# Kernel optimization log

Hardware: AMD Instinct MI355X
Metric: run time of the kernel (lower is better)

Reference implementation:

```python
import jax, jax.numpy as jnp
import numpy as np

B, S, D, H = 2, 2048, 1024, 16
HD = D // H
MASK_VALUE = -1000000.0


def setup_inputs() -> dict:
    key = jax.random.key(0)
    ks = jax.random.split(key, 8)
    scale = 1.0 / np.sqrt(D)
    return {
        "Q": jax.random.normal(ks[0], (B, S, D), jnp.float32),
        "K": jax.random.normal(ks[1], (B, S, D), jnp.float32),
        "V": jax.random.normal(ks[2], (B, S, D), jnp.float32),
        "valid_lens": jax.random.randint(ks[3], (B,), 0, S).astype(jnp.int32),
        "Wq": jax.random.normal(ks[4], (D, D), jnp.float32) * scale,
        "Wk": jax.random.normal(ks[5], (D, D), jnp.float32) * scale,
        "Wv": jax.random.normal(ks[6], (D, D), jnp.float32) * scale,
        "Wo": jax.random.normal(ks[7], (D, D), jnp.float32) * scale,
    }


def _split_heads(x):
    # [B,S,D] -> [B,H,S,HD]
    return x.reshape(B, S, H, HD).transpose(0, 2, 1, 3)


def reference(Q, K, V, valid_lens, Wq, Wk, Wv, Wo):
    q = _split_heads(Q @ Wq)
    k = _split_heads(K @ Wk)
    v = _split_heads(V @ Wv)
    # scores: [B,H,Sq,Sk]
    scores = jnp.einsum("bhqd,bhkd->bhqk", q, k) / jnp.sqrt(jnp.float32(HD))
    # mask key positions >= valid_len (per batch, broadcast over heads/queries)
    key_pos = jnp.arange(S)  # [Sk]
    mask = key_pos[None, None, None, :] < valid_lens[:, None, None, None]
    scores = jnp.where(mask, scores, MASK_VALUE)
    attn = jax.nn.softmax(scores, axis=-1)
    out = jnp.einsum("bhqk,bhkd->bhqd", attn, v)  # [B,H,S,HD]
    out = out.transpose(0, 2, 1, 3).reshape(B, S, D)
    return out @ Wo
```

## Files before the change

kernel.cpp:

```cpp
#include <hip/hip_runtime.h>
#include <stdint.h>

#define B_ 2
#define S_ 2048
#define D_ 1024
#define H_ 16
#define HD_ 64
#define MG_ (B_*S_)
#define MASKV -1000000.0f
#define LDA_ 72

typedef __bf16 bf16;
typedef bf16 bf16x8 __attribute__((ext_vector_type(8)));
typedef bf16 bf16x4 __attribute__((ext_vector_type(4)));
typedef float f32x4 __attribute__((ext_vector_type(4)));

#define MFMA(a, b, c) __builtin_amdgcn_mfma_f32_16x16x32_bf16(a, b, c, 0, 0, 0)

__global__ __launch_bounds__(256) void wcast_kernel(const float* __restrict__ W0, const float* __restrict__ W1,
                                                    const float* __restrict__ W2, const float* __restrict__ W3,
                                                    bf16* __restrict__ T) {
  const float* W = blockIdx.z == 0 ? W0 : blockIdx.z == 1 ? W1 : blockIdx.z == 2 ? W2 : W3;
  bf16* Tz = T + (size_t)blockIdx.z * D_ * D_;
  __shared__ float tile[32][33];
  int tx = threadIdx.x & 31, ty = threadIdx.x >> 5;
  int bn = blockIdx.x * 32, bk = blockIdx.y * 32;
#pragma unroll
  for (int i = 0; i < 32; i += 8)
    tile[ty + i][tx] = W[(size_t)(bk + ty + i) * D_ + bn + tx];
  __syncthreads();
#pragma unroll
  for (int i = 0; i < 32; i += 8)
    Tz[(size_t)(bn + ty + i) * D_ + bk + tx] = (bf16)tile[tx][ty + i];
}

__global__ __launch_bounds__(256) void proj_gemm(const float* __restrict__ Qin, const float* __restrict__ Kin,
                                                 const float* __restrict__ Vin, const bf16* __restrict__ WT,
                                                 bf16* __restrict__ qh, bf16* __restrict__ kh,
                                                 bf16* __restrict__ vT) {
  __shared__ alignas(16) bf16 As[128 * 32];
  __shared__ alignas(16) bf16 Bs[128 * 32];
  int mode = blockIdx.z;
  int tid = threadIdx.x, lane = tid & 63, w = tid >> 6;
  int wm = w >> 1, wn = w & 1, ml = lane & 15, quad = lane >> 4;
  int rr = tid >> 3, c4 = (tid & 7) * 4;
  f32x4 acc[4][4] = {};

  if (mode < 2) {
    const float* A = mode ? Kin : Qin;
    const bf16* Bt = WT + (size_t)mode * D_ * D_;
    bf16* dst = mode ? kh : qh;
    int m0 = blockIdx.y * 128, n0 = blockIdx.x * 128;
    for (int kk = 0; kk < D_; kk += 32) {
      __syncthreads();
#pragma unroll
      for (int p = 0; p < 4; ++p) {
        float4 v = *(const float4*)&A[(size_t)(m0 + rr + p * 32) * D_ + kk + c4];
        bf16x4 bv; bv[0] = (bf16)v.x; bv[1] = (bf16)v.y; bv[2] = (bf16)v.z; bv[3] = (bf16)v.w;
        *(bf16x4*)&As[(rr + p * 32) * 32 + c4] = bv;
      }
#pragma unroll
      for (int p = 0; p < 2; ++p) {
        int cc = tid + p * 256;
        int nr = cc >> 2, c8 = (cc & 3) * 8;
        *(bf16x8*)&Bs[nr * 32 + c8] = *(const bf16x8*)&Bt[(size_t)(n0 + nr) * D_ + kk + c8];
      }
      __syncthreads();
      bf16x8 af[4], bfr[4];
#pragma unroll
      for (int mt = 0; mt < 4; ++mt) af[mt] = *(bf16x8*)&As[(wm * 64 + mt * 16 + ml) * 32 + quad * 8];
#pragma unroll
      for (int nt = 0; nt < 4; ++nt) bfr[nt] = *(bf16x8*)&Bs[(wn * 64 + nt * 16 + ml) * 32 + quad * 8];
#pragma unroll
      for (int mt = 0; mt < 4; ++mt)
#pragma unroll
        for (int nt = 0; nt < 4; ++nt)
          acc[mt][nt] = MFMA(af[mt], bfr[nt], acc[mt][nt]);
    }
#pragma unroll
    for (int mt = 0; mt < 4; ++mt)
#pragma unroll
      for (int nt = 0; nt < 4; ++nt)
#pragma unroll
        for (int r = 0; r < 4; ++r) {
          int m = m0 + wm * 64 + mt * 16 + quad * 4 + r;
          int n = n0 + wn * 64 + nt * 16 + ml;
          int b = m >> 11, s = m & (S_ - 1), h = n >> 6, hd = n & 63;
          dst[(((size_t)(b * H_ + h)) * S_ + s) * HD_ + hd] = (bf16)acc[mt][nt][r];
        }
  } else {
    const bf16* At = WT + 2ull * D_ * D_;
    int m0 = blockIdx.x * 128;
    int n0 = blockIdx.y * 128;
    for (int kk = 0; kk < D_; kk += 32) {
      __syncthreads();
#pragma unroll
      for (int p = 0; p < 2; ++p) {
        int cc = tid + p * 256;
        int nr = cc >> 2, c8 = (cc & 3) * 8;
        *(bf16x8*)&As[nr * 32 + c8] = *(const bf16x8*)&At[(size_t)(m0 + nr) * D_ + kk + c8];
      }
#pragma unroll
      for (int p = 0; p < 4; ++p) {
        float4 v = *(const float4*)&Vin[(size_t)(n0 + rr + p * 32) * D_ + kk + c4];
        bf16x4 bv; bv[0] = (bf16)v.x; bv[1] = (bf16)v.y; bv[2] = (bf16)v.z; bv[3] = (bf16)v.w;
        *(bf16x4*)&Bs[(rr + p * 32) * 32 + c4] = bv;
      }
      __syncthreads();
      bf16x8 af[4], bfr[4];
#pragma unroll
      for (int mt = 0; mt < 4; ++mt) af[mt] = *(bf16x8*)&As[(wm * 64 + mt * 16 + ml) * 32 + quad * 8];
#pragma unroll
      for (int nt = 0; nt < 4; ++nt) bfr[nt] = *(bf16x8*)&Bs[(wn * 64 + nt * 16 + ml) * 32 + quad * 8];
#pragma unroll
      for (int mt = 0; mt < 4; ++mt)
#pragma unroll
        for (int nt = 0; nt < 4; ++nt)
          acc[mt][nt] = MFMA(af[mt], bfr[nt], acc[mt][nt]);
    }
#pragma unroll
    for (int mt = 0; mt < 4; ++mt)
#pragma unroll
      for (int nt = 0; nt < 4; ++nt)
#pragma unroll
        for (int r = 0; r < 4; ++r) {
          int dcol = m0 + wm * 64 + mt * 16 + quad * 4 + r;
          int n = n0 + wn * 64 + nt * 16 + ml;
          int b = n >> 11, s = n & (S_ - 1), h = dcol >> 6, hd = dcol & 63;
          vT[(((size_t)(b * H_ + h)) * HD_ + hd) * S_ + s] = (bf16)acc[mt][nt][r];
        }
  }
}

__global__ __launch_bounds__(256) void attn_kernel(const bf16* __restrict__ qh, const bf16* __restrict__ kh,
                                                   const bf16* __restrict__ vT, const int* __restrict__ vlen,
                                                   bf16* __restrict__ ctx) {
  __shared__ alignas(16) bf16 Qs[64 * LDA_];
  __shared__ alignas(16) bf16 Ks[64 * LDA_];
  __shared__ alignas(16) bf16 Vs[64 * LDA_];
  __shared__ alignas(16) bf16 Ps[4][16 * LDA_];
  int tid = threadIdx.x, lane = tid & 63, w = tid >> 6;
  int ml = lane & 15, quad = lane >> 4;
  int bh = blockIdx.y, b = bh >> 4, h = bh & 15;
  int qt = blockIdx.x;
  const bf16* qbase = qh + ((size_t)bh * S_ + qt * 64) * HD_;
  const bf16* kbase = kh + (size_t)bh * S_ * HD_;
  const bf16* vbase = vT + (size_t)bh * HD_ * S_;
  int valid = vlen[b];
  int nkt = (valid == 0) ? (S_ / 64) : ((valid + 63) >> 6);
  for (int c = tid; c < 64 * 8; c += 256) {
    int r = c >> 3, c8 = (c & 7) * 8;
    *(bf16x8*)&Qs[r * LDA_ + c8] = *(const bf16x8*)&qbase[r * 64 + c8];
  }
  float m_run[4] = {-1e30f, -1e30f, -1e30f, -1e30f};
  float l_run[4] = {0.f, 0.f, 0.f, 0.f};
  f32x4 o[4] = {};
  for (int kt = 0; kt < nkt; ++kt) {
    __syncthreads();
    for (int c = tid; c < 64 * 8; c += 256) {
      int r = c >> 3, c8 = (c & 7) * 8;
      *(bf16x8*)&Ks[r * LDA_ + c8] = *(const bf16x8*)&kbase[((size_t)kt * 64 + r) * HD_ + c8];
      *(bf16x8*)&Vs[r * LDA_ + c8] = *(const bf16x8*)&vbase[(size_t)r * S_ + kt * 64 + c8];
    }
    __syncthreads();
    bf16x8 aq0 = *(bf16x8*)&Qs[(w * 16 + ml) * LDA_ + quad * 8];
    bf16x8 aq1 = *(bf16x8*)&Qs[(w * 16 + ml) * LDA_ + 32 + quad * 8];
    f32x4 sc[4];
#pragma unroll
    for (int nt = 0; nt < 4; ++nt) {
      bf16x8 bk0 = *(bf16x8*)&Ks[(nt * 16 + ml) * LDA_ + quad * 8];
      bf16x8 bk1 = *(bf16x8*)&Ks[(nt * 16 + ml) * LDA_ + 32 + quad * 8];
      f32x4 c = {};
      c = MFMA(aq0, bk0, c);
      c = MFMA(aq1, bk1, c);
      sc[nt] = c;
    }
#pragma unroll
    for (int r = 0; r < 4; ++r) {
      float mx = -1e30f;
#pragma unroll
      for (int nt = 0; nt < 4; ++nt) {
        float s = sc[nt][r] * 0.125f;
        int col = kt * 64 + nt * 16 + ml;
        if (col >= valid) s = MASKV;
        sc[nt][r] = s;
        mx = fmaxf(mx, s);
      }
#pragma unroll
      for (int d = 1; d < 16; d <<= 1) mx = fmaxf(mx, __shfl_xor(mx, d));
      float mnew = fmaxf(m_run[r], mx);
      float ps = 0.f;
#pragma unroll
      for (int nt = 0; nt < 4; ++nt) {
        float p = __expf(sc[nt][r] - mnew);
        sc[nt][r] = p;
        ps += p;
      }
#pragma unroll
      for (int d = 1; d < 16; d <<= 1) ps += __shfl_xor(ps, d);
      float alpha = __expf(m_run[r] - mnew);
      l_run[r] = l_run[r] * alpha + ps;
      m_run[r] = mnew;
      o[0][r] *= alpha; o[1][r] *= alpha; o[2][r] *= alpha; o[3][r] *= alpha;
#pragma unroll
      for (int nt = 0; nt < 4; ++nt)
        Ps[w][(quad * 4 + r) * LDA_ + nt * 16 + ml] = (bf16)sc[nt][r];
    }
#pragma unroll
    for (int ks = 0; ks < 2; ++ks) {
      bf16x8 ap = *(bf16x8*)&Ps[w][ml * LDA_ + ks * 32 + quad * 8];
#pragma unroll
      for (int ht = 0; ht < 4; ++ht) {
        bf16x8 bv = *(bf16x8*)&Vs[(ht * 16 + ml) * LDA_ + ks * 32 + quad * 8];
        o[ht] = MFMA(ap, bv, o[ht]);
      }
    }
  }
#pragma unroll
  for (int r = 0; r < 4; ++r) {
    float inv = 1.0f / l_run[r];
    int s = qt * 64 + w * 16 + quad * 4 + r;
#pragma unroll
    for (int ht = 0; ht < 4; ++ht) {
      int d = h * 64 + ht * 16 + ml;
      ctx[((size_t)b * S_ + s) * D_ + d] = (bf16)(o[ht][r] * inv);
    }
  }
}

__global__ __launch_bounds__(256) void out_gemm(const bf16* __restrict__ ctx, const bf16* __restrict__ WoT,
                                                float* __restrict__ out) {
  __shared__ alignas(16) bf16 As[128 * 32];
  __shared__ alignas(16) bf16 Bs[64 * 32];
  int tid = threadIdx.x, lane = tid & 63, w = tid >> 6;
  int wm = w >> 1, wn = w & 1, ml = lane & 15, quad = lane >> 4;
  int m0 = blockIdx.y * 128, n0 = blockIdx.x * 64;
  f32x4 acc[4][2] = {};
  for (int kk = 0; kk < D_; kk += 32) {
    __syncthreads();
    {
#pragma unroll
      for (int p = 0; p < 2; ++p) {
        int cc = tid + p * 256;
        int nr = cc >> 2, c8 = (cc & 3) * 8;
        *(bf16x8*)&As[nr * 32 + c8] = *(const bf16x8*)&ctx[(size_t)(m0 + nr) * D_ + kk + c8];
      }
      int nr = tid >> 2, c8 = (tid & 3) * 8;
      *(bf16x8*)&Bs[nr * 32 + c8] = *(const bf16x8*)&WoT[(size_t)(n0 + nr) * D_ + kk + c8];
    }
    __syncthreads();
    bf16x8 af[4], bfr[2];
#pragma unroll
    for (int mt = 0; mt < 4; ++mt) af[mt] = *(bf16x8*)&As[(wm * 64 + mt * 16 + ml) * 32 + quad * 8];
#pragma unroll
    for (int nt = 0; nt < 2; ++nt) bfr[nt] = *(bf16x8*)&Bs[(wn * 32 + nt * 16 + ml) * 32 + quad * 8];
#pragma unroll
    for (int mt = 0; mt < 4; ++mt)
#pragma unroll
      for (int nt = 0; nt < 2; ++nt)
        acc[mt][nt] = MFMA(af[mt], bfr[nt], acc[mt][nt]);
  }
#pragma unroll
  for (int mt = 0; mt < 4; ++mt)
#pragma unroll
    for (int nt = 0; nt < 2; ++nt)
#pragma unroll
      for (int r = 0; r < 4; ++r) {
        int m = m0 + wm * 64 + mt * 16 + quad * 4 + r;
        int n = n0 + wn * 32 + nt * 16 + ml;
        out[(size_t)m * D_ + n] = acc[mt][nt][r];
      }
}

extern "C" void kernel_launch(void* const* d_in, const int* in_sizes, int n_in,
                              void* d_out, int out_size, void* d_ws, size_t ws_size,
                              hipStream_t stream) {
  const float* Q = (const float*)d_in[0];
  const float* K = (const float*)d_in[1];
  const float* V = (const float*)d_in[2];
  const int* vl = (const int*)d_in[3];
  const float* Wq = (const float*)d_in[4];
  const float* Wk = (const float*)d_in[5];
  const float* Wv = (const float*)d_in[6];
  const float* Wo = (const float*)d_in[7];
  char* ws = (char*)d_ws;
  bf16* WT  = (bf16*)ws;
  bf16* qh  = (bf16*)(ws + 8ull * 1024 * 1024);
  bf16* kh  = (bf16*)(ws + 16ull * 1024 * 1024);
  bf16* vT  = (bf16*)(ws + 24ull * 1024 * 1024);
  bf16* ctx = (bf16*)(ws + 32ull * 1024 * 1024);
  float* out = (float*)d_out;

  wcast_kernel<<<dim3(32, 32, 4), 256, 0, stream>>>(Wq, Wk, Wv, Wo, WT);
  proj_gemm<<<dim3(D_ / 128, MG_ / 128, 3), 256, 0, stream>>>(Q, K, V, WT, qh, kh, vT);
  attn_kernel<<<dim3(S_ / 64, B_ * H_), 256, 0, stream>>>(qh, kh, vT, vl, ctx);
  out_gemm<<<dim3(D_ / 64, MG_ / 128), 256, 0, stream>>>(ctx, WT + 3ull * D_ * D_, out);
}
```

Measured before the change: 249.7 us.

## Split attention key range across warps and merge partial softmax in LDS

The attention kernel now has each warp handle 32 query rows over half of the key tiles (even or odd), loading Q, K and V fragments straight from global memory into registers instead of staging them in shared memory with block-wide barriers. The per-warp partial outputs, maxima and sums are written to LDS at the end and combined split-k style. The 1/sqrt(d) scale is folded into the Q projection epilogue, and the mask check runs only on tail tiles. This removes the per-tile __syncthreads and LDS staging in exchange for redundant global K/V loads across warps and an extra merge step at the end.

```diff
diff --git a/kernel.cpp b/kernel.cpp
--- a/kernel.cpp
+++ b/kernel.cpp
@@ -8,7 +8,8 @@
 #define HD_ 64
 #define MG_ (B_*S_)
 #define MASKV -1000000.0f
-#define LDA_ 72
+#define LP_ 72
+#define LO_ 68
 
 typedef __bf16 bf16;
 typedef bf16 bf16x8 __attribute__((ext_vector_type(8)));
@@ -50,6 +51,7 @@
     const float* A = mode ? Kin : Qin;
     const bf16* Bt = WT + (size_t)mode * D_ * D_;
     bf16* dst = mode ? kh : qh;
+    float oscale = mode ? 1.0f : 0.125f;
     int m0 = blockIdx.y * 128, n0 = blockIdx.x * 128;
     for (int kk = 0; kk < D_; kk += 32) {
       __syncthreads();
@@ -86,7 +88,7 @@
           int m = m0 + wm * 64 + mt * 16 + quad * 4 + r;
           int n = n0 + wn * 64 + nt * 16 + ml;
           int b = m >> 11, s = m & (S_ - 1), h = n >> 6, hd = n & 63;
-          dst[(((size_t)(b * H_ + h)) * S_ + s) * HD_ + hd] = (bf16)acc[mt][nt][r];
+          dst[(((size_t)(b * H_ + h)) * S_ + s) * HD_ + hd] = (bf16)(acc[mt][nt][r] * oscale);
         }
   } else {
     const bf16* At = WT + 2ull * D_ * D_;
@@ -135,96 +137,136 @@
 __global__ __launch_bounds__(256) void attn_kernel(const bf16* __restrict__ qh, const bf16* __restrict__ kh,
                                                    const bf16* __restrict__ vT, const int* __restrict__ vlen,
                                                    bf16* __restrict__ ctx) {
-  __shared__ alignas(16) bf16 Qs[64 * LDA_];
-  __shared__ alignas(16) bf16 Ks[64 * LDA_];
-  __shared__ alignas(16) bf16 Vs[64 * LDA_];
-  __shared__ alignas(16) bf16 Ps[4][16 * LDA_];
+  __shared__ alignas(16) char ldsraw[35840];
+  bf16* Ps = (bf16*)ldsraw;
+  float* Om = (float*)ldsraw;
+  float* Mv = (float*)(ldsraw + 34816);
+  float* Lv = (float*)(ldsraw + 35328);
+
   int tid = threadIdx.x, lane = tid & 63, w = tid >> 6;
   int ml = lane & 15, quad = lane >> 4;
+  int wq = w >> 1, wk = w & 1;
   int bh = blockIdx.y, b = bh >> 4, h = bh & 15;
   int qt = blockIdx.x;
-  const bf16* qbase = qh + ((size_t)bh * S_ + qt * 64) * HD_;
+  const bf16* qbase = qh + ((size_t)bh * S_ + qt * 64 + wq * 32) * HD_;
   const bf16* kbase = kh + (size_t)bh * S_ * HD_;
   const bf16* vbase = vT + (size_t)bh * HD_ * S_;
   int valid = vlen[b];
   int nkt = (valid == 0) ? (S_ / 64) : ((valid + 63) >> 6);
-  for (int c = tid; c < 64 * 8; c += 256) {
-    int r = c >> 3, c8 = (c & 7) * 8;
-    *(bf16x8*)&Qs[r * LDA_ + c8] = *(const bf16x8*)&qbase[r * 64 + c8];
-  }
-  float m_run[4] = {-1e30f, -1e30f, -1e30f, -1e30f};
-  float l_run[4] = {0.f, 0.f, 0.f, 0.f};
-  f32x4 o[4] = {};
-  for (int kt = 0; kt < nkt; ++kt) {
-    __syncthreads();
-    for (int c = tid; c < 64 * 8; c += 256) {
-      int r = c >> 3, c8 = (c & 7) * 8;
-      *(bf16x8*)&Ks[r * LDA_ + c8] = *(const bf16x8*)&kbase[((size_t)kt * 64 + r) * HD_ + c8];
-      *(bf16x8*)&Vs[r * LDA_ + c8] = *(const bf16x8*)&vbase[(size_t)r * S_ + kt * 64 + c8];
-    }
-    __syncthreads();
-    bf16x8 aq0 = *(bf16x8*)&Qs[(w * 16 + ml) * LDA_ + quad * 8];
-    bf16x8 aq1 = *(bf16x8*)&Qs[(w * 16 + ml) * LDA_ + 32 + quad * 8];
-    f32x4 sc[4];
-#pragma unroll
-    for (int nt = 0; nt < 4; ++nt) {
-      bf16x8 bk0 = *(bf16x8*)&Ks[(nt * 16 + ml) * LDA_ + quad * 8];
-      bf16x8 bk1 = *(bf16x8*)&Ks[(nt * 16 + ml) * LDA_ + 32 + quad * 8];
-      f32x4 c = {};
-      c = MFMA(aq0, bk0, c);
-      c = MFMA(aq1, bk1, c);
-      sc[nt] = c;
-    }
+
+  bf16x8 aq[2][2];
+#pragma unroll
+  for (int mt = 0; mt < 2; ++mt)
+#pragma unroll
+    for (int half = 0; half < 2; ++half)
+      aq[mt][half] = *(const bf16x8*)&qbase[(mt * 16 + ml) * HD_ + half * 32 + quad * 8];
+
+  float m_run[2][4], l_run[2][4];
+#pragma unroll
+  for (int mt = 0; mt < 2; ++mt)
+#pragma unroll
+    for (int r = 0; r < 4; ++r) { m_run[mt][r] = -1e30f; l_run[mt][r] = 0.f; }
+  f32x4 o[2][4] = {};
+
+  bf16* Pw = Ps + (size_t)w * 32 * LP_;
+
+  for (int kt = wk; kt < nkt; kt += 2) {
+    const bf16* kp = kbase + (size_t)kt * 64 * HD_;
+    bool tail = (kt * 64 + 64 > valid);
+    bf16x8 bk[4][2];
+#pragma unroll
+    for (int nt = 0; nt < 4; ++nt)
+#pragma unroll
+      for (int half = 0; half < 2; ++half)
+        bk[nt][half] = *(const bf16x8*)&kp[(nt * 16 + ml) * HD_ + half * 32 + quad * 8];
+
+#pragma unroll
+    for (int mt = 0; mt < 2; ++mt) {
+      f32x4 sc[4];
+#pragma unroll
+      for (int nt = 0; nt < 4; ++nt) {
+        f32x4 c = {};
+        c = MFMA(aq[mt][0], bk[nt][0], c);
+        c = MFMA(aq[mt][1], bk[nt][1], c);
+        sc[nt] = c;
+      }
+#pragma unroll
+      for (int r = 0; r < 4; ++r) {
+        float mx = -1e30f;
+#pragma unroll
+        for (int nt = 0; nt < 4; ++nt) {
+          float s = sc[nt][r];
+          if (tail) {
+            int col = kt * 64 + nt * 16 + ml;
+            if (col >= valid) s = MASKV;
+          }
+          sc[nt][r] = s;
+          mx = fmaxf(mx, s);
+        }
+#pragma unroll
+        for (int d = 1; d < 16; d <<= 1) mx = fmaxf(mx, __shfl_xor(mx, d));
+        float mnew = fmaxf(m_run[mt][r], mx);
+        float ps = 0.f;
+#pragma unroll
+        for (int nt = 0; nt < 4; ++nt) {
+          float p = __expf(sc[nt][r] - mnew);
+          sc[nt][r] = p;
+          ps += p;
+        }
+#pragma unroll
+        for (int d = 1; d < 16; d <<= 1) ps += __shfl_xor(ps, d);
+        float alpha = __expf(m_run[mt][r] - mnew);
+        l_run[mt][r] = l_run[mt][r] * alpha + ps;
+        m_run[mt][r] = mnew;
+#pragma unroll
+        for (int ht = 0; ht < 4; ++ht) o[mt][ht][r] *= alpha;
+#pragma unroll
+        for (int nt = 0; nt < 4; ++nt)
+          Pw[(mt * 16 + quad * 4 + r) * LP_ + nt * 16 + ml] = (bf16)sc[nt][r];
+      }
+    }
+#pragma unroll
+    for (int ks = 0; ks < 2; ++ks) {
+      bf16x8 bv[4];
+#pragma unroll
+      for (int ht = 0; ht < 4; ++ht)
+        bv[ht] = *(const bf16x8*)&vbase[(size_t)(ht * 16 + ml) * S_ + kt * 64 + ks * 32 + quad * 8];
+#pragma unroll
+      for (int mt = 0; mt < 2; ++mt) {
+        bf16x8 ap = *(bf16x8*)&Pw[(mt * 16 + ml) * LP_ + ks * 32 + quad * 8];
+#pragma unroll
+        for (int ht = 0; ht < 4; ++ht) o[mt][ht] = MFMA(ap, bv[ht], o[mt][ht]);
+      }
+    }
+  }
+
+  __syncthreads();
+#pragma unroll
+  for (int mt = 0; mt < 2; ++mt) {
 #pragma unroll
     for (int r = 0; r < 4; ++r) {
-      float mx = -1e30f;
-#pragma unroll
-      for (int nt = 0; nt < 4; ++nt) {
-        float s = sc[nt][r] * 0.125f;
-        int col = kt * 64 + nt * 16 + ml;
-        if (col >= valid) s = MASKV;
-        sc[nt][r] = s;
-        mx = fmaxf(mx, s);
-      }
-#pragma unroll
-      for (int d = 1; d < 16; d <<= 1) mx = fmaxf(mx, __shfl_xor(mx, d));
-      float mnew = fmaxf(m_run[r], mx);
-      float ps = 0.f;
-#pragma unroll
-      for (int nt = 0; nt < 4; ++nt) {
-        float p = __expf(sc[nt][r] - mnew);
-        sc[nt][r] = p;
-        ps += p;
-      }
-#pragma unroll
-      for (int d = 1; d < 16; d <<= 1) ps += __shfl_xor(ps, d);
-      float alpha = __expf(m_run[r] - mnew);
-      l_run[r] = l_run[r] * alpha + ps;
-      m_run[r] = mnew;
-      o[0][r] *= alpha; o[1][r] *= alpha; o[2][r] *= alpha; o[3][r] *= alpha;
-#pragma unroll
-      for (int nt = 0; nt < 4; ++nt)
-        Ps[w][(quad * 4 + r) * LDA_ + nt * 16 + ml] = (bf16)sc[nt][r];
-    }
-#pragma unroll
-    for (int ks = 0; ks < 2; ++ks) {
-      bf16x8 ap = *(bf16x8*)&Ps[w][ml * LDA_ + ks * 32 + quad * 8];
-#pragma unroll
-      for (int ht = 0; ht < 4; ++ht) {
-        bf16x8 bv = *(bf16x8*)&Vs[(ht * 16 + ml) * LDA_ + ks * 32 + quad * 8];
-        o[ht] = MFMA(ap, bv, o[ht]);
-      }
-    }
-  }
-#pragma unroll
-  for (int r = 0; r < 4; ++r) {
-    float inv = 1.0f / l_run[r];
-    int s = qt * 64 + w * 16 + quad * 4 + r;
-#pragma unroll
-    for (int ht = 0; ht < 4; ++ht) {
-      int d = h * 64 + ht * 16 + ml;
-      ctx[((size_t)b * S_ + s) * D_ + d] = (bf16)(o[ht][r] * inv);
-    }
+      int rl = mt * 16 + quad * 4 + r;
+#pragma unroll
+      for (int ht = 0; ht < 4; ++ht)
+        Om[(w * 32 + rl) * LO_ + ht * 16 + ml] = o[mt][ht][r];
+      if (ml == 0) {
+        Mv[w * 32 + rl] = m_run[mt][r];
+        Lv[w * 32 + rl] = l_run[mt][r];
+      }
+    }
+  }
+  __syncthreads();
+#pragma unroll 4
+  for (int rr = 0; rr < 16; ++rr) {
+    int rg = w * 16 + rr;
+    int wqs = rg >> 5, rl = rg & 31;
+    int s0 = (wqs * 2) * 32 + rl, s1 = (wqs * 2 + 1) * 32 + rl;
+    float ma = Mv[s0], mb = Mv[s1];
+    float ms = fmaxf(ma, mb);
+    float ca = __expf(ma - ms), cb = __expf(mb - ms);
+    float ls = ca * Lv[s0] + cb * Lv[s1];
+    float ov = ca * Om[s0 * LO_ + lane] + cb * Om[s1 * LO_ + lane];
+    ctx[((size_t)b * S_ + qt * 64 + rg) * D_ + h * 64 + lane] = (bf16)(ov / ls);
   }
 }
 
```

Measured after the change: 243.6 us. -2.5%, faster.
